# Kernel tuning notes

Measured on AMD Instinct MI355X. Metric: run time of the kernel, lower is better.

## Reference

```python
import jax, jax.numpy as jnp
import numpy as np

T, B, D, H = 512, 256, 64, 128  # timesteps, num_envs, obs_dim, lstm hidden


def setup_inputs() -> dict:
    key = jax.random.key(0)
    ks = jax.random.split(key, 8)
    x = jax.random.normal(ks[0], (T, B, D), dtype=jnp.float32)
    done = (jax.random.uniform(ks[1], (T, B)) < 0.02).astype(jnp.float32)
    h0 = 0.01 * jax.random.normal(ks[2], (B, H), dtype=jnp.float32)
    c0 = 0.01 * jax.random.normal(ks[3], (B, H), dtype=jnp.float32)
    W_ih = jax.random.normal(ks[4], (4 * H, D), dtype=jnp.float32) / np.sqrt(D)
    W_hh = jax.random.normal(ks[5], (4 * H, H), dtype=jnp.float32) / np.sqrt(H)
    b_ih = jnp.zeros((4 * H,), dtype=jnp.float32)
    b_hh = jnp.zeros((4 * H,), dtype=jnp.float32)
    W_hid = jax.random.normal(ks[6], (H, H), dtype=jnp.float32) * np.sqrt(2.0 / H)
    b_hid = jnp.zeros((H,), dtype=jnp.float32)
    return {"x": x, "done": done, "h0": h0, "c0": c0,
            "W_ih": W_ih, "b_ih": b_ih, "W_hh": W_hh, "b_hh": b_hh,
            "W_hid": W_hid, "b_hid": b_hid}


def reference(x, done, h0, c0, W_ih, b_ih, W_hh, b_hh, W_hid, b_hid):
    # Precompute input contribution to gates for all timesteps: [T, B, 4H]
    xg = jnp.einsum('tbd,gd->tbg', x, W_ih) + b_ih + b_hh

    def step(carry, inp):
        h, c = carry            # [B, H] each
        xg_t, d = inp           # [B, 4H], [B]
        mask = (1.0 - d)[:, None]
        h = h * mask            # reset state where episode ended
        c = c * mask
        gates = xg_t + h @ W_hh.T            # [B, 4H]
        i, f, g, o = jnp.split(gates, 4, axis=-1)  # PyTorch gate order i,f,g,o
        c = jax.nn.sigmoid(f) * c + jax.nn.sigmoid(i) * jnp.tanh(g)
        h = jax.nn.sigmoid(o) * jnp.tanh(c)
        return (h, c), h

    (_, _), hs = jax.lax.scan(step, (h0, c0), (xg, done))  # hs: [T, B, H]
    hidden = hs.reshape(-1, H) @ W_hid.T + b_hid           # [T*B, H]
    return hidden
```

## Files before the change

### kernel.cpp

```cpp
#include <hip/hip_runtime.h>

#define T_STEPS 512
#define B_ENV   256
#define D_IN    64
#define H_DIM   128
#define G4      512

typedef _Float16 h2v __attribute__((ext_vector_type(2)));
typedef _Float16 h8v __attribute__((ext_vector_type(8)));
typedef float    f4v __attribute__((ext_vector_type(4)));

__device__ __forceinline__ float dot2(h2v a, h2v b, float c) {
#if __has_builtin(__builtin_amdgcn_fdot2)
    return __builtin_amdgcn_fdot2(a, b, c, false);
#else
    return c + (float)a.x * (float)b.x + (float)a.y * (float)b.y;
#endif
}

__device__ __forceinline__ h2v pack16(float a, float b) {
#if __has_builtin(__builtin_amdgcn_cvt_pkrtz)
    union { __fp16 __attribute__((ext_vector_type(2))) r; h2v h; } u;
    u.r = __builtin_amdgcn_cvt_pkrtz(a, b);
    return u.h;
#else
    h2v p; p.x = (_Float16)a; p.y = (_Float16)b; return p;
#endif
}

__device__ __forceinline__ float fast_rcp(float x) {
#if __has_builtin(__builtin_amdgcn_rcpf)
    return __builtin_amdgcn_rcpf(x);
#else
    return 1.0f / x;
#endif
}
__device__ __forceinline__ float sigm(float x)   { return fast_rcp(1.0f + __expf(-x)); }
__device__ __forceinline__ float tanh_f(float x) { float e = __expf(2.0f * x); return 1.0f - 2.0f * fast_rcp(e + 1.0f); }

template <int CTRL>
__device__ __forceinline__ float dpp_mov(float v) {
    int s = __builtin_amdgcn_update_dpp(
        0, __builtin_bit_cast(int, v), CTRL, 0xF, 0xF, true);
    return __builtin_bit_cast(float, s);
}
__device__ __forceinline__ float quad_allreduce(float v) {
    v += dpp_mov<0xB1>(v);
    v += dpp_mov<0x4E>(v);
    return v;
}

__device__ __forceinline__ void sync_lds() {
    asm volatile("s_waitcnt lgkmcnt(0)" ::: "memory");
    __builtin_amdgcn_s_barrier();
    asm volatile("" ::: "memory");
}

__device__ __forceinline__ void async_load_row(const float* gsrc, float* ldst) {
    __builtin_amdgcn_global_load_lds(
        (const __attribute__((address_space(1))) unsigned int*)gsrc,
        (__attribute__((address_space(3))) unsigned int*)ldst, 4, 0, 0);
}

__global__ __launch_bounds__(512, 2)
void ppo_lstm_scan(const float* __restrict__ x,
                   const float* __restrict__ done,
                   const float* __restrict__ h0,
                   const float* __restrict__ c0,
                   const float* __restrict__ W_ih,
                   const float* __restrict__ b_ih,
                   const float* __restrict__ W_hh,
                   const float* __restrict__ b_hh,
                   float* __restrict__ hs)
{
    const int b    = blockIdx.x;
    const int tid  = threadIdx.x;
    const int lane = tid & 63;
    const int wid  = tid >> 6;
    const int qq   = tid & 3;
    const int j    = tid >> 2;

    __shared__ alignas(16) h2v   h16[2][H_DIM / 2];
    __shared__ alignas(16) h2v   x16[2][D_IN / 2];
    __shared__ alignas(16) float smask[T_STEPS];
    __shared__ alignas(16) float xring[4][D_IN];

    h2v whh[64];
    h2v wih[32];
    #pragma unroll
    for (int g = 0; g < 4; ++g) {
        const float* wr = W_hh + (size_t)(g * H_DIM + j) * H_DIM + qq * 32;
        #pragma unroll
        for (int c = 0; c < 16; ++c)
            whh[g * 16 + c] = pack16(wr[2 * c], wr[2 * c + 1]);
        const float* wr2 = W_ih + (size_t)(g * H_DIM + j) * D_IN + qq * 16;
        #pragma unroll
        for (int c = 0; c < 8; ++c)
            wih[g * 8 + c] = pack16(wr2[2 * c], wr2[2 * c + 1]);
    }
    const int   r_own    = qq * H_DIM + j;
    const float bias_own = b_ih[r_own] + b_hh[r_own];
    float       c_reg    = c0[b * H_DIM + j];

    smask[tid] = 1.0f - done[(size_t)tid * B_ENV + b];
    if (tid < 64) {
        const float sm0 = 1.0f - done[b];
        const float* hp = h0 + b * H_DIM;
        h16[0][tid] = pack16(hp[2 * tid] * sm0, hp[2 * tid + 1] * sm0);
    }
    if (wid == 0) {
        #pragma unroll
        for (int s = 0; s < 3; ++s)
            async_load_row(x + ((size_t)s * B_ENV + b) * D_IN + lane, &xring[s][0]);
    }
    __syncthreads();
    if (wid == 0 && lane < 32) {
        float2 v = *reinterpret_cast<const float2*>(&xring[0][2 * lane]);
        x16[0][lane] = pack16(v.x, v.y);
    }
    sync_lds();

    for (int t = 0; t < T_STEPS; ++t) {
        const int rb = t & 1, wb = rb ^ 1;

        if (wid == 0) {
            const int t3 = (t + 3 < T_STEPS) ? (t + 3) : (T_STEPS - 1);
            async_load_row(x + ((size_t)t3 * B_ENV + b) * D_IN + lane,
                           &xring[(t + 3) & 3][0]);
            if (lane < 32) {
                float2 v = *reinterpret_cast<const float2*>(
                    &xring[(t + 1) & 3][2 * lane]);
                x16[wb][lane] = pack16(v.x, v.y);
            }
        }

        const h8v* hp8 = reinterpret_cast<const h8v*>(&h16[rb][qq * 16]);
        const h8v* xp8 = reinterpret_cast<const h8v*>(&x16[rb][qq * 8]);
        float s0 = 0.f, s1 = 0.f, s2 = 0.f, s3 = 0.f;
        #pragma unroll
        for (int c4 = 0; c4 < 4; ++c4) {
            union { h8v v; h2v p[4]; } u;
            u.v = hp8[c4];
            #pragma unroll
            for (int pp = 0; pp < 4; ++pp) {
                s0 = dot2(whh[      c4 * 4 + pp], u.p[pp], s0);
                s1 = dot2(whh[16 +  c4 * 4 + pp], u.p[pp], s1);
                s2 = dot2(whh[32 +  c4 * 4 + pp], u.p[pp], s2);
                s3 = dot2(whh[48 +  c4 * 4 + pp], u.p[pp], s3);
            }
        }
        #pragma unroll
        for (int c4 = 0; c4 < 2; ++c4) {
            union { h8v v; h2v p[4]; } u;
            u.v = xp8[c4];
            #pragma unroll
            for (int pp = 0; pp < 4; ++pp) {
                s0 = dot2(wih[      c4 * 4 + pp], u.p[pp], s0);
                s1 = dot2(wih[ 8 +  c4 * 4 + pp], u.p[pp], s1);
                s2 = dot2(wih[16 +  c4 * 4 + pp], u.p[pp], s2);
                s3 = dot2(wih[24 +  c4 * 4 + pp], u.p[pp], s3);
            }
        }

        s0 = quad_allreduce(s0);
        s1 = quad_allreduce(s1);
        s2 = quad_allreduce(s2);
        s3 = quad_allreduce(s3);

        const float s01 = (qq & 1) ? s1 : s0;
        const float s23 = (qq & 1) ? s3 : s2;
        const float gs  = ((qq & 2) ? s23 : s01) + bias_own;
        const float av  = (qq == 2) ? tanh_f(gs) : sigm(gs);
        const float ai  = dpp_mov<0x00>(av);
        const float af  = dpp_mov<0x55>(av);
        const float ag  = dpp_mov<0xAA>(av);
        const float ao  = dpp_mov<0xFF>(av);

        const float dm = smask[t];
        const float cn = af * (c_reg * dm) + ai * ag;
        c_reg = cn;
        const float hn = ao * tanh_f(cn);

        if (wid == 0) {
            asm volatile("s_waitcnt vmcnt(1)" ::: "memory");
        }
        if (qq == 0) {
            const float smn = smask[(t + 1 < T_STEPS) ? (t + 1) : (T_STEPS - 1)];
            reinterpret_cast<_Float16*>(h16[wb])[j] = (_Float16)(hn * smn);
            hs[((size_t)t * B_ENV + b) * H_DIM + j] = hn;
        }
        sync_lds();
    }
}

#define PADK 68
__global__ __launch_bounds__(256)
void ppo_proj(const float* __restrict__ W_hid,
              const float* __restrict__ b_hid,
              float* __restrict__ out)
{
    __shared__ h2v wl[H_DIM][PADK];
    __shared__ h2v hl[H_DIM][PADK];
    const int tid = threadIdx.x;
    const int rg  = tid >> 4;
    const int cg  = tid & 15;

    const size_t r0 = (size_t)blockIdx.x * H_DIM;

    #pragma unroll
    for (int i = 0; i < 16; ++i) {
        const int idx = tid + 256 * i;
        const int r = idx >> 5, cc = idx & 31;
        f4v v = *reinterpret_cast<const f4v*>(W_hid + 4 * (size_t)idx);
        wl[r][2 * cc]     = pack16(v.x, v.y);
        wl[r][2 * cc + 1] = pack16(v.z, v.w);
    }
    #pragma unroll
    for (int i = 0; i < 16; ++i) {
        const int idx = tid + 256 * i;
        const int r = idx >> 5, cc = idx & 31;
        f4v v = *reinterpret_cast<const f4v*>(out + (r0 + r) * H_DIM + 4 * cc);
        hl[r][2 * cc]     = pack16(v.x, v.y);
        hl[r][2 * cc + 1] = pack16(v.z, v.w);
    }
    float bcol[8];
    #pragma unroll
    for (int jj = 0; jj < 8; ++jj) bcol[jj] = b_hid[cg + 16 * jj];
    __syncthreads();

    float acc[8][8];
    #pragma unroll
    for (int i = 0; i < 8; ++i)
        #pragma unroll
        for (int jj = 0; jj < 8; ++jj) acc[i][jj] = 0.f;

    for (int kq = 0; kq < 16; ++kq) {
        union { h8v v; h2v p[4]; } hv[8], wv[8];
        #pragma unroll
        for (int i = 0; i < 8; ++i)
            hv[i].v = *reinterpret_cast<const h8v*>(&hl[rg * 8 + i][4 * kq]);
        #pragma unroll
        for (int jj = 0; jj < 8; ++jj)
            wv[jj].v = *reinterpret_cast<const h8v*>(&wl[cg + 16 * jj][4 * kq]);
        #pragma unroll
        for (int i = 0; i < 8; ++i)
            #pragma unroll
            for (int jj = 0; jj < 8; ++jj) {
                acc[i][jj] = dot2(hv[i].p[0], wv[jj].p[0], acc[i][jj]);
                acc[i][jj] = dot2(hv[i].p[1], wv[jj].p[1], acc[i][jj]);
                acc[i][jj] = dot2(hv[i].p[2], wv[jj].p[2], acc[i][jj]);
                acc[i][jj] = dot2(hv[i].p[3], wv[jj].p[3], acc[i][jj]);
            }
    }

    #pragma unroll
    for (int i = 0; i < 8; ++i)
        #pragma unroll
        for (int jj = 0; jj < 8; ++jj)
            out[(r0 + rg * 8 + i) * H_DIM + cg + 16 * jj] = acc[i][jj] + bcol[jj];
}

extern "C" void kernel_launch(void* const* d_in, const int* in_sizes, int n_in,
                              void* d_out, int out_size, void* d_ws, size_t ws_size,
                              hipStream_t stream) {
    const float* x     = (const float*)d_in[0];
    const float* done  = (const float*)d_in[1];
    const float* h0    = (const float*)d_in[2];
    const float* c0    = (const float*)d_in[3];
    const float* W_ih  = (const float*)d_in[4];
    const float* b_ih  = (const float*)d_in[5];
    const float* W_hh  = (const float*)d_in[6];
    const float* b_hh  = (const float*)d_in[7];
    const float* W_hid = (const float*)d_in[8];
    const float* b_hid = (const float*)d_in[9];
    float* out = (float*)d_out;
    (void)d_ws; (void)ws_size; (void)out_size; (void)n_in; (void)in_sizes;

    hipLaunchKernelGGL(ppo_lstm_scan, dim3(B_ENV), dim3(512), 0, stream,
                       x, done, h0, c0, W_ih, b_ih, W_hh, b_hh, out);
    hipLaunchKernelGGL(ppo_proj, dim3((T_STEPS * B_ENV) / H_DIM), dim3(256), 0, stream,
                       W_hid, b_hid, out);
}
```

Measured before the change: 445.6 us.

## Pack two environments per 1024-thread block in LSTM scan kernel

```diff
diff --git a/kernel.cpp b/kernel.cpp
--- a/kernel.cpp
+++ b/kernel.cpp
@@ -62,7 +62,7 @@
         (__attribute__((address_space(3))) unsigned int*)ldst, 4, 0, 0);
 }
 
-__global__ __launch_bounds__(512, 2)
+__global__ __launch_bounds__(1024, 4)
 void ppo_lstm_scan(const float* __restrict__ x,
                    const float* __restrict__ done,
                    const float* __restrict__ h0,
@@ -73,17 +73,19 @@
                    const float* __restrict__ b_hh,
                    float* __restrict__ hs)
 {
-    const int b    = blockIdx.x;
     const int tid  = threadIdx.x;
+    const int half = tid >> 9;
+    const int l    = tid & 511;
+    const int b    = blockIdx.x * 2 + half;
     const int lane = tid & 63;
-    const int wid  = tid >> 6;
-    const int qq   = tid & 3;
-    const int j    = tid >> 2;
-
-    __shared__ alignas(16) h2v   h16[2][H_DIM / 2];
-    __shared__ alignas(16) h2v   x16[2][D_IN / 2];
-    __shared__ alignas(16) float smask[T_STEPS];
-    __shared__ alignas(16) float xring[4][D_IN];
+    const int lwid = (tid >> 6) & 7;
+    const int qq   = l & 3;
+    const int j    = l >> 2;
+
+    __shared__ alignas(16) h2v   h16[2][2][H_DIM / 2];
+    __shared__ alignas(16) h2v   x16[2][2][D_IN / 2];
+    __shared__ alignas(16) float smask[2][T_STEPS];
+    __shared__ alignas(16) float xring[2][4][D_IN];
 
     h2v whh[64];
     h2v wih[32];
@@ -102,40 +104,41 @@
     const float bias_own = b_ih[r_own] + b_hh[r_own];
     float       c_reg    = c0[b * H_DIM + j];
 
-    smask[tid] = 1.0f - done[(size_t)tid * B_ENV + b];
-    if (tid < 64) {
+    smask[half][l] = 1.0f - done[(size_t)l * B_ENV + b];
+    if (l < 64) {
         const float sm0 = 1.0f - done[b];
         const float* hp = h0 + b * H_DIM;
-        h16[0][tid] = pack16(hp[2 * tid] * sm0, hp[2 * tid + 1] * sm0);
-    }
-    if (wid == 0) {
+        h16[half][0][l] = pack16(hp[2 * l] * sm0, hp[2 * l + 1] * sm0);
+    }
+    if (lwid == 0) {
         #pragma unroll
         for (int s = 0; s < 3; ++s)
-            async_load_row(x + ((size_t)s * B_ENV + b) * D_IN + lane, &xring[s][0]);
+            async_load_row(x + ((size_t)s * B_ENV + b) * D_IN + lane,
+                           &xring[half][s][0]);
     }
     __syncthreads();
-    if (wid == 0 && lane < 32) {
-        float2 v = *reinterpret_cast<const float2*>(&xring[0][2 * lane]);
-        x16[0][lane] = pack16(v.x, v.y);
+    if (lwid == 0 && lane < 32) {
+        float2 v = *reinterpret_cast<const float2*>(&xring[half][0][2 * lane]);
+        x16[half][0][lane] = pack16(v.x, v.y);
     }
     sync_lds();
 
     for (int t = 0; t < T_STEPS; ++t) {
         const int rb = t & 1, wb = rb ^ 1;
 
-        if (wid == 0) {
+        if (lwid == 0) {
             const int t3 = (t + 3 < T_STEPS) ? (t + 3) : (T_STEPS - 1);
             async_load_row(x + ((size_t)t3 * B_ENV + b) * D_IN + lane,
-                           &xring[(t + 3) & 3][0]);
+                           &xring[half][(t + 3) & 3][0]);
             if (lane < 32) {
                 float2 v = *reinterpret_cast<const float2*>(
-                    &xring[(t + 1) & 3][2 * lane]);
-                x16[wb][lane] = pack16(v.x, v.y);
-            }
-        }
-
-        const h8v* hp8 = reinterpret_cast<const h8v*>(&h16[rb][qq * 16]);
-        const h8v* xp8 = reinterpret_cast<const h8v*>(&x16[rb][qq * 8]);
+                    &xring[half][(t + 1) & 3][2 * lane]);
+                x16[half][wb][lane] = pack16(v.x, v.y);
+            }
+        }
+
+        const h8v* hp8 = reinterpret_cast<const h8v*>(&h16[half][rb][qq * 16]);
+        const h8v* xp8 = reinterpret_cast<const h8v*>(&x16[half][rb][qq * 8]);
         float s0 = 0.f, s1 = 0.f, s2 = 0.f, s3 = 0.f;
         #pragma unroll
         for (int c4 = 0; c4 < 4; ++c4) {
@@ -176,17 +179,17 @@
         const float ag  = dpp_mov<0xAA>(av);
         const float ao  = dpp_mov<0xFF>(av);
 
-        const float dm = smask[t];
+        const float dm = smask[half][t];
         const float cn = af * (c_reg * dm) + ai * ag;
         c_reg = cn;
         const float hn = ao * tanh_f(cn);
 
-        if (wid == 0) {
+        if (lwid == 0) {
             asm volatile("s_waitcnt vmcnt(1)" ::: "memory");
         }
         if (qq == 0) {
-            const float smn = smask[(t + 1 < T_STEPS) ? (t + 1) : (T_STEPS - 1)];
-            reinterpret_cast<_Float16*>(h16[wb])[j] = (_Float16)(hn * smn);
+            const float smn = smask[half][(t + 1 < T_STEPS) ? (t + 1) : (T_STEPS - 1)];
+            reinterpret_cast<_Float16*>(h16[half][wb])[j] = (_Float16)(hn * smn);
             hs[((size_t)t * B_ENV + b) * H_DIM + j] = hn;
         }
         sync_lds();
@@ -276,7 +279,7 @@
     float* out = (float*)d_out;
     (void)d_ws; (void)ws_size; (void)out_size; (void)n_in; (void)in_sizes;
 
-    hipLaunchKernelGGL(ppo_lstm_scan, dim3(B_ENV), dim3(512), 0, stream,
+    hipLaunchKernelGGL(ppo_lstm_scan, dim3(B_ENV / 2), dim3(1024), 0, stream,
                        x, done, h0, c0, W_ih, b_ih, W_hh, b_hh, out);
     hipLaunchKernelGGL(ppo_proj, dim3((T_STEPS * B_ENV) / H_DIM), dim3(256), 0, stream,
                        W_hid, b_hid, out);
```

New measurement: 703.6 us. 57.9% more time.

## Load x directly into registers with one-step prefetch instead of LDS ring

Applied to the files above, without the earlier changes.

```diff
diff --git a/kernel.cpp b/kernel.cpp
--- a/kernel.cpp
+++ b/kernel.cpp
@@ -56,13 +56,7 @@
     asm volatile("" ::: "memory");
 }
 
-__device__ __forceinline__ void async_load_row(const float* gsrc, float* ldst) {
-    __builtin_amdgcn_global_load_lds(
-        (const __attribute__((address_space(1))) unsigned int*)gsrc,
-        (__attribute__((address_space(3))) unsigned int*)ldst, 4, 0, 0);
-}
-
-__global__ __launch_bounds__(512, 2)
+__global__ __launch_bounds__(512, 1) __attribute__((amdgpu_waves_per_eu(2, 2)))
 void ppo_lstm_scan(const float* __restrict__ x,
                    const float* __restrict__ done,
                    const float* __restrict__ h0,
@@ -73,17 +67,13 @@
                    const float* __restrict__ b_hh,
                    float* __restrict__ hs)
 {
-    const int b    = blockIdx.x;
-    const int tid  = threadIdx.x;
-    const int lane = tid & 63;
-    const int wid  = tid >> 6;
-    const int qq   = tid & 3;
-    const int j    = tid >> 2;
+    const int b   = blockIdx.x;
+    const int tid = threadIdx.x;
+    const int qq  = tid & 3;
+    const int j   = tid >> 2;
 
     __shared__ alignas(16) h2v   h16[2][H_DIM / 2];
-    __shared__ alignas(16) h2v   x16[2][D_IN / 2];
     __shared__ alignas(16) float smask[T_STEPS];
-    __shared__ alignas(16) float xring[4][D_IN];
 
     h2v whh[64];
     h2v wih[32];
@@ -108,34 +98,33 @@
         const float* hp = h0 + b * H_DIM;
         h16[0][tid] = pack16(hp[2 * tid] * sm0, hp[2 * tid + 1] * sm0);
     }
-    if (wid == 0) {
-        #pragma unroll
-        for (int s = 0; s < 3; ++s)
-            async_load_row(x + ((size_t)s * B_ENV + b) * D_IN + lane, &xring[s][0]);
+    f4v xr[4];
+    {
+        const float* xp = x + (size_t)b * D_IN + qq * 16;
+        #pragma unroll
+        for (int i = 0; i < 4; ++i)
+            xr[i] = *reinterpret_cast<const f4v*>(xp + 4 * i);
     }
     __syncthreads();
-    if (wid == 0 && lane < 32) {
-        float2 v = *reinterpret_cast<const float2*>(&xring[0][2 * lane]);
-        x16[0][lane] = pack16(v.x, v.y);
-    }
-    sync_lds();
 
     for (int t = 0; t < T_STEPS; ++t) {
         const int rb = t & 1, wb = rb ^ 1;
 
-        if (wid == 0) {
-            const int t3 = (t + 3 < T_STEPS) ? (t + 3) : (T_STEPS - 1);
-            async_load_row(x + ((size_t)t3 * B_ENV + b) * D_IN + lane,
-                           &xring[(t + 3) & 3][0]);
-            if (lane < 32) {
-                float2 v = *reinterpret_cast<const float2*>(
-                    &xring[(t + 1) & 3][2 * lane]);
-                x16[wb][lane] = pack16(v.x, v.y);
-            }
+        h2v xh[8];
+        #pragma unroll
+        for (int i = 0; i < 4; ++i) {
+            xh[2 * i]     = pack16(xr[i].x, xr[i].y);
+            xh[2 * i + 1] = pack16(xr[i].z, xr[i].w);
+        }
+        {
+            const int tn = (t + 1 < T_STEPS) ? (t + 1) : t;
+            const float* xp = x + ((size_t)tn * B_ENV + b) * D_IN + qq * 16;
+            #pragma unroll
+            for (int i = 0; i < 4; ++i)
+                xr[i] = *reinterpret_cast<const f4v*>(xp + 4 * i);
         }
 
         const h8v* hp8 = reinterpret_cast<const h8v*>(&h16[rb][qq * 16]);
-        const h8v* xp8 = reinterpret_cast<const h8v*>(&x16[rb][qq * 8]);
         float s0 = 0.f, s1 = 0.f, s2 = 0.f, s3 = 0.f;
         #pragma unroll
         for (int c4 = 0; c4 < 4; ++c4) {
@@ -150,16 +139,11 @@
             }
         }
         #pragma unroll
-        for (int c4 = 0; c4 < 2; ++c4) {
-            union { h8v v; h2v p[4]; } u;
-            u.v = xp8[c4];
-            #pragma unroll
-            for (int pp = 0; pp < 4; ++pp) {
-                s0 = dot2(wih[      c4 * 4 + pp], u.p[pp], s0);
-                s1 = dot2(wih[ 8 +  c4 * 4 + pp], u.p[pp], s1);
-                s2 = dot2(wih[16 +  c4 * 4 + pp], u.p[pp], s2);
-                s3 = dot2(wih[24 +  c4 * 4 + pp], u.p[pp], s3);
-            }
+        for (int c = 0; c < 8; ++c) {
+            s0 = dot2(wih[     c], xh[c], s0);
+            s1 = dot2(wih[ 8 + c], xh[c], s1);
+            s2 = dot2(wih[16 + c], xh[c], s2);
+            s3 = dot2(wih[24 + c], xh[c], s3);
         }
 
         s0 = quad_allreduce(s0);
@@ -181,9 +165,6 @@
         c_reg = cn;
         const float hn = ao * tanh_f(cn);
 
-        if (wid == 0) {
-            asm volatile("s_waitcnt vmcnt(1)" ::: "memory");
-        }
         if (qq == 0) {
             const float smn = smask[(t + 1 < T_STEPS) ? (t + 1) : (T_STEPS - 1)];
             reinterpret_cast<_Float16*>(h16[wb])[j] = (_Float16)(hn * smn);
```

After: 462.5 us. 3.8% more time.
